# Kernel tuning notes

Measured on AMD Instinct MI355X. Metric: run time of the kernel, lower is better.

Reference implementation:

```python
import jax, jax.numpy as jnp
import numpy as np

B, S, D = 8, 4096, 192
MEM_READ, MEM_WRITE, MEM_READY = 156, 157, 158


def setup_inputs() -> dict:
    key = jax.random.key(0)
    ks = jax.random.split(key, 9)
    inp = {"x": jax.random.normal(ks[0], (B, S, D), dtype=jnp.float32)}
    names = ["Wq_r", "Wk_r", "Wv_r", "Wo_r", "Wq_w", "Wk_w", "Wv_w", "Wo_w"]
    for i, n in enumerate(names):
        inp[n] = jax.random.normal(ks[i + 1], (D, D), dtype=jnp.float32) * 0.02
    return inp


def _attention(x, Wq, Wk, Wv, Wo):
    # single-head, non-causal PureAttention: q/k/v = x @ W.T, softmax(qk^T/sqrt(D)) v, then W_o
    q = jnp.einsum('bsd,ed->bse', x, Wq)
    k = jnp.einsum('bsd,ed->bse', x, Wk)
    v = jnp.einsum('bsd,ed->bse', x, Wv)
    scale = jnp.asarray(1.0 / np.sqrt(D), x.dtype)
    scores = jnp.einsum('bqe,bke->bqk', q, k) * scale  # [B,S,S]
    attn = jax.nn.softmax(scores, axis=-1)
    o = jnp.einsum('bqk,bke->bqe', attn, v)
    return jnp.einsum('bse,oe->bso', o, Wo)


def reference(x, Wq_r, Wk_r, Wv_r, Wo_r, Wq_w, Wk_w, Wv_w, Wo_w):
    read_flag = x[:, 0, MEM_READ]    # [B]
    write_flag = x[:, 0, MEM_WRITE]  # [B]
    read_res = _attention(x, Wq_r, Wk_r, Wv_r, Wo_r)
    write_res = _attention(x, Wq_w, Wk_w, Wv_w, Wo_w)
    rg = read_flag[:, None, None]
    wg = write_flag[:, None, None]
    out = x + rg * (read_res - x) + wg * (write_res - x)
    out = out.at[:, :, MEM_READ].set(0.0)
    out = out.at[:, :, MEM_WRITE].set(0.0)
    ready = (read_flag + write_flag)[:, None]  # broadcast over seq
    out = out.at[:, :, MEM_READY].set(jnp.broadcast_to(ready, out.shape[:2]))
    return out
```

## Files before the change

### kernel.cpp

```cpp
#include <hip/hip_runtime.h>
#include <stdint.h>

#define B_ 8
#define S_ 4096
#define D_ 192
#define M_ (B_*S_)
#define VTILE 13824
#define KTILE 12800
#define NT_ 64

typedef short v8s __attribute__((ext_vector_type(8)));
typedef float v4f __attribute__((ext_vector_type(4)));
typedef unsigned long long ull;

static __device__ __forceinline__ unsigned short f2bf(float f){
  union{float f; unsigned u;} v; v.f=f;
  unsigned u = v.u;
  unsigned r = (u + 0x7fffu + ((u>>16)&1u))>>16;
  return (unsigned short)r;
}
static __device__ __forceinline__ float fexp2(float x){
  return __builtin_amdgcn_exp2f(x);
}

static __device__ __forceinline__ unsigned sw_fp8(float x){
  union{float f; unsigned u;} v; v.f = x;
  unsigned s = (v.u >> 24) & 0x80u;
  float a = fabsf(x);
  if (a < 0.001953125f) return s;
  if (a >= 240.f) return s | 0x7Eu;
  if (a < 0.015625f) {
    int m = (int)(a*512.f + 0.5f); if(m>7) m=7;
    return s | (unsigned)m;
  }
  int e = (int)((v.u >> 23) & 0xff) - 127;
  unsigned mant = (v.u >> 20) & 0x7u;
  unsigned rest = v.u & 0xFFFFFu;
  if (rest > 0x80000u || (rest == 0x80000u && (mant&1u))) mant++;
  unsigned ee = (unsigned)(e + 7);
  if (mant == 8u){ mant = 0u; ee++; }
  return s | (ee<<3) | mant;
}
template<bool HI>
static __device__ __forceinline__ unsigned pk8(float a, float b, unsigned old){
#if __has_builtin(__builtin_amdgcn_cvt_pk_fp8_f32)
  return __builtin_amdgcn_cvt_pk_fp8_f32(a, b, old, HI);
#else
  unsigned p = sw_fp8(a) | (sw_fp8(b)<<8);
  return HI ? ((old & 0x0000FFFFu) | (p<<16)) : ((old & 0xFFFF0000u) | p);
#endif
}

typedef const __attribute__((address_space(1))) unsigned int gu32;
typedef __attribute__((address_space(3))) unsigned int lu32;
#define GLL16(gp, lp) __builtin_amdgcn_global_load_lds((gu32*)(gp), (lu32*)(lp), 16, 0, 0)

__global__ void cvt_w_kernel(const float* w0,const float* w1,const float* w2,const float* w3,
                             const float* w4,const float* w5,const float* w6,const float* w7,
                             unsigned short* dst){
  int w = blockIdx.y;
  const float* src;
  switch(w){
    case 0: src=w0; break; case 1: src=w1; break; case 2: src=w2; break; case 3: src=w3; break;
    case 4: src=w4; break; case 5: src=w5; break; case 6: src=w6; break; default: src=w7; break;
  }
  int i = blockIdx.x*256 + threadIdx.x;
  float v = src[i];
  if(w==0 || w==4 || w==1 || w==5) v *= 0.32267249f;
  dst[(size_t)w*36864 + i] = f2bf(v);
}

__global__ __launch_bounds__(256) void proj_kernel(
    const float* __restrict__ x, const unsigned short* __restrict__ Wb,
    unsigned char* __restrict__ Q8g, unsigned char* __restrict__ K8t,
    unsigned char* __restrict__ V8)
{
  __shared__ __align__(16) unsigned char Vstage8[VTILE];
  const size_t MDB = (size_t)M_*D_;
  int path = blockIdx.y;
  int tid = threadIdx.x;
  int wid = tid>>6, lane = tid&63;
  int lr = lane&15, lg = lane>>4, kb = lg*8;
  int m0 = blockIdx.x*64 + wid*16;
  int row = m0 + lr;

  v8s a[6];
  #pragma unroll
  for(int c=0;c<6;c++){
    const float* xp = &x[(size_t)row*D_ + c*32 + kb];
    float4 f0 = *(const float4*)xp;
    float4 f1 = *(const float4*)(xp+4);
    v8s t;
    t[0]=(short)f2bf(f0.x); t[1]=(short)f2bf(f0.y); t[2]=(short)f2bf(f0.z); t[3]=(short)f2bf(f0.w);
    t[4]=(short)f2bf(f1.x); t[5]=(short)f2bf(f1.y); t[6]=(short)f2bf(f1.z); t[7]=(short)f2bf(f1.w);
    a[c]=t;
  }
  int bidx = m0 / S_;
  int sb   = (blockIdx.x*64) % S_;
  int tile = sb >> 6;
  int sloc = wid*16 + lg*4;

  {
    const unsigned short* W = Wb + (size_t)(path*4 + 0)*36864;
    unsigned char* dst = Q8g + (size_t)path*MDB;
    #pragma unroll
    for(int nt=0; nt<12; nt++){
      v4f acc = {0.f,0.f,0.f,0.f};
      int n = nt*16 + lr;
      #pragma unroll
      for(int c=0;c<6;c++){
        v8s bfr = *(const v8s*)&W[(size_t)n*D_ + c*32 + kb];
        acc = __builtin_amdgcn_mfma_f32_16x16x32_bf16(a[c], bfr, acc, 0,0,0);
      }
      int col = nt*16 + lr;
      int r0 = m0 + lg*4;
      #pragma unroll
      for(int r=0;r<4;r++){
        unsigned p = pk8<false>(acc[r], 0.f, 0u);
        dst[(size_t)(r0+r)*D_ + col] = (unsigned char)(p & 0xFF);
      }
    }
  }
  {
    const unsigned short* W = Wb + (size_t)(path*4 + 1)*36864;
    unsigned char* dstK = K8t + (((size_t)path*B_ + bidx)*NT_ + tile)*KTILE;
    #pragma unroll
    for(int nt=0; nt<12; nt++){
      v4f acc = {0.f,0.f,0.f,0.f};
      int n = nt*16 + lr;
      #pragma unroll
      for(int c=0;c<6;c++){
        v8s bfr = *(const v8s*)&W[(size_t)n*D_ + c*32 + kb];
        acc = __builtin_amdgcn_mfma_f32_16x16x32_bf16(a[c], bfr, acc, 0,0,0);
      }
      int col = nt*16 + lr;
      #pragma unroll
      for(int r=0;r<4;r++){
        unsigned p = pk8<false>(acc[r], 0.f, 0u);
        dstK[(size_t)(sloc+r)*200 + col] = (unsigned char)(p & 0xFF);
      }
    }
  }
  {
    const unsigned short* W = Wb + (size_t)(path*4 + 2)*36864;
    #pragma unroll
    for(int nt=0; nt<12; nt++){
      v4f acc = {0.f,0.f,0.f,0.f};
      int n = nt*16 + lr;
      #pragma unroll
      for(int c=0;c<6;c++){
        v8s bfr = *(const v8s*)&W[(size_t)n*D_ + c*32 + kb];
        acc = __builtin_amdgcn_mfma_f32_16x16x32_bf16(a[c], bfr, acc, 0,0,0);
      }
      int col = nt*16 + lr;
      unsigned pk4 = pk8<false>(acc[0], acc[1], 0u);
      pk4 = pk8<true>(acc[2], acc[3], pk4);
      *(unsigned*)&Vstage8[col*72 + sloc] = pk4;
    }
    __syncthreads();
    unsigned char* dstV = V8 + (((size_t)path*B_ + bidx)*NT_ + tile)*VTILE;
    #pragma unroll
    for(int j=0;j<4;j++){
      int i = tid + j*256;
      if(i<864) *(v8s*)&dstV[i*16] = *(const v8s*)&Vstage8[i*16];
    }
  }
}

__global__ __launch_bounds__(512,4) void attn_kernel(
    const unsigned char* __restrict__ Q8g,
    const unsigned char* __restrict__ K8t,
    const unsigned char* __restrict__ V8,
    unsigned short* __restrict__ Ob)
{
  __shared__ __align__(16) unsigned char KL[2][KTILE];
  __shared__ __align__(16) unsigned char VL8[3][VTILE];

  int flat = blockIdx.x + 32*blockIdx.y + 256*blockIdx.z;
  int w = (flat&7)*64 + (flat>>3);
  int qi = w & 31;
  int b  = (w>>5) & 7;
  int z  = w>>8;

  const size_t MDB = (size_t)M_*D_;
  const unsigned char* Q8 = Q8g + (size_t)z*MDB;
  const unsigned char* Kp = K8t + ((size_t)z*B_ + b)*NT_*KTILE;
  const unsigned char* Vp = V8 + ((size_t)z*B_ + b)*NT_*VTILE;
  unsigned short* O = Ob + (size_t)z*MDB;

  int q0 = qi*128;
  int tid = threadIdx.x, wid=tid>>6, lane=tid&63;
  int lr = lane&15, lg = lane>>4;
  size_t bK = (size_t)b*S_*D_;
  int qrow0 = q0 + wid*16;

  long qf8[6];
  {
    const unsigned char* qp = Q8 + bK + (size_t)(qrow0 + lr)*D_;
    #pragma unroll
    for(int c=0;c<6;c++) qf8[c] = *(const long*)(qp + c*32 + lg*8);
  }
  float lsum = 0.f;
  v4f oacc[12];
  #pragma unroll
  for(int e=0;e<12;e++) oacc[e] = (v4f){0.f,0.f,0.f,0.f};

  bool k2 = tid < 288;
  bool v2 = tid < 352;

  auto stage = [&](int t, int kbuf, int vbuf){
    const unsigned char* kg = Kp + (size_t)t*KTILE;
    const unsigned char* vg = Vp + (size_t)t*VTILE;
    GLL16(kg + tid*16, &KL[kbuf][tid*16]);
    if(k2) GLL16(kg + (512+tid)*16, &KL[kbuf][(512+tid)*16]);
    GLL16(vg + tid*16, &VL8[vbuf][tid*16]);
    if(v2) GLL16(vg + (512+tid)*16, &VL8[vbuf][(512+tid)*16]);
  };
  auto do_qk = [&](int kcur, v4f sacc[4]){
    __builtin_amdgcn_s_setprio(1);
    #pragma unroll
    for(int ct=0; ct<4; ct++){
      v4f s = {0.f,0.f,0.f,0.f};
      const unsigned char* rb = &KL[kcur][(ct*16+lr)*200];
      #pragma unroll
      for(int c=0;c<6;c++){
        long kf8 = *(const long*)(rb + c*32 + lg*8);
        s = __builtin_amdgcn_mfma_f32_16x16x32_fp8_fp8(kf8, qf8[c], s, 0,0,0);
      }
      sacc[ct]=s;
    }
    __builtin_amdgcn_s_setprio(0);
  };
  auto do_softmax = [&](v4f sacc[4], long pa8[2]){
    #pragma unroll
    for(int h=0; h<2; h++){
      v4f s0 = sacc[2*h], s1 = sacc[2*h+1];
      float p00=fexp2(s0[0]), p01=fexp2(s0[1]), p02=fexp2(s0[2]), p03=fexp2(s0[3]);
      float p10=fexp2(s1[0]), p11=fexp2(s1[1]), p12=fexp2(s1[2]), p13=fexp2(s1[3]);
      lsum += ((p00+p01)+(p02+p03)) + ((p10+p11)+(p12+p13));
      unsigned A = pk8<false>(p00,p01,0u); A = pk8<true>(p02,p03,A);
      unsigned Bx= pk8<false>(p10,p11,0u); Bx= pk8<true>(p12,p13,Bx);
      asm("v_permlane32_swap_b32 %0, %1" : "+v"(Bx), "+v"(A));
      asm("v_permlane16_swap_b32 %0, %1" : "+v"(Bx), "+v"(A));
      pa8[h] = (long)(((ull)Bx<<32) | (ull)A);
    }
  };
  auto do_pv = [&](int vcur, long pa8[2]){
    __builtin_amdgcn_s_setprio(1);
    #pragma unroll
    for(int e=0;e<12;e++){
      const unsigned char* vr = &VL8[vcur][(e*16+lr)*72 + lg*8];
      long vb0 = *(const long*)(vr);
      long vb1 = *(const long*)(vr + 32);
      oacc[e] = __builtin_amdgcn_mfma_f32_16x16x32_fp8_fp8(pa8[0], vb0, oacc[e], 0,0,0);
      oacc[e] = __builtin_amdgcn_mfma_f32_16x16x32_fp8_fp8(pa8[1], vb1, oacc[e], 0,0,0);
    }
    __builtin_amdgcn_s_setprio(0);
  };

  stage(0, 0, 0);
  asm volatile("s_waitcnt vmcnt(0)" ::: "memory");
  __syncthreads();

  long pa_prev[2];
  {
    v4f sacc[4];
    do_qk(0, sacc);
    stage(1, 1, 1);
    __builtin_amdgcn_sched_barrier(0);
    do_softmax(sacc, pa_prev);
    asm volatile("s_waitcnt vmcnt(0)" ::: "memory");
    __syncthreads();
  }

  for(int t=1; t<NT_; t++){
    v4f sacc[4];
    do_qk(t&1, sacc);
    if(t<NT_-1) stage(t+1, (t+1)&1, (t+1)%3);
    __builtin_amdgcn_sched_barrier(0);
    do_pv((t-1)%3, pa_prev);
    do_softmax(sacc, pa_prev);
    asm volatile("s_waitcnt vmcnt(0)" ::: "memory");
    __syncthreads();
  }
  do_pv((NT_-1)%3, pa_prev);

  float ps = lsum;
  ps += __shfl_xor(ps, 16);
  ps += __shfl_xor(ps, 32);
  float iv = 1.0f/ps;
  float invr[4];
  #pragma unroll
  for(int r=0;r<4;r++) invr[r] = __shfl(iv, lg*4+r, 16);
  size_t orow0 = ((size_t)b*S_ + qrow0 + lg*4)*D_;
  #pragma unroll
  for(int e=0;e<12;e++){
    #pragma unroll
    for(int r=0;r<4;r++){
      O[orow0 + (size_t)r*D_ + e*16 + lr] = f2bf(oacc[e][r]*invr[r]);
    }
  }
}

__global__ __launch_bounds__(256) void final_kernel(
  const float* __restrict__ x,
  const unsigned short* __restrict__ Or,
  const unsigned short* __restrict__ Ow,
  const unsigned short* __restrict__ WoR,
  const unsigned short* __restrict__ WoW,
  float* __restrict__ out)
{
  int halfn = blockIdx.y;
  int tid=threadIdx.x, wid=tid>>6, lane=tid&63;
  int lr=lane&15, lg=lane>>4, kb=lg*8;
  int m0 = blockIdx.x*64 + wid*16;
  int arow = m0 + lr;
  v8s ar[6], aw[6];
  #pragma unroll
  for(int c=0;c<6;c++){
    ar[c] = *(const v8s*)&Or[(size_t)arow*D_ + c*32 + kb];
    aw[c] = *(const v8s*)&Ow[(size_t)arow*D_ + c*32 + kb];
  }
  int bidx = m0 / S_;
  float rf = x[(size_t)bidx*S_*D_ + 156];
  float wf = x[(size_t)bidx*S_*D_ + 157];
  #pragma unroll
  for(int ntl=0; ntl<6; ntl++){
    int nt = halfn*6 + ntl;
    v4f accR={0.f,0.f,0.f,0.f}, accW={0.f,0.f,0.f,0.f};
    int n = nt*16 + lr;
    #pragma unroll
    for(int c=0;c<6;c++){
      v8s br = *(const v8s*)&WoR[(size_t)n*D_ + c*32 + kb];
      accR = __builtin_amdgcn_mfma_f32_16x16x32_bf16(ar[c], br, accR,0,0,0);
      v8s bw = *(const v8s*)&WoW[(size_t)n*D_ + c*32 + kb];
      accW = __builtin_amdgcn_mfma_f32_16x16x32_bf16(aw[c], bw, accW,0,0,0);
    }
    #pragma unroll
    for(int r=0;r<4;r++){
      int row = m0 + lg*4 + r;
      int col = nt*16 + lr;
      float xv = x[(size_t)row*D_ + col];
      float val = xv + rf*(accR[r]-xv) + wf*(accW[r]-xv);
      if(col==156||col==157) val = 0.f;
      else if(col==158) val = rf+wf;
      out[(size_t)row*D_ + col] = val;
    }
  }
}

extern "C" void kernel_launch(void* const* d_in, const int* in_sizes, int n_in,
                              void* d_out, int out_size, void* d_ws, size_t ws_size,
                              hipStream_t stream) {
  const float* x = (const float*)d_in[0];
  char* wsb = (char*)d_ws;
  const size_t WSZ = 36864;
  const size_t MDB = (size_t)M_*D_;
  const size_t K8SZ = (size_t)2*B_*NT_*KTILE;
  const size_t V8SZ = (size_t)2*B_*NT_*VTILE;
  unsigned short* Wb  = (unsigned short*)wsb;
  unsigned char*  Q8  = (unsigned char*)(wsb + 8*WSZ*2);
  unsigned char*  K8t = Q8 + 2*MDB;
  unsigned char*  V8  = K8t + K8SZ;
  unsigned short* Ob  = (unsigned short*)(V8 + V8SZ);

  cvt_w_kernel<<<dim3(144,8),256,0,stream>>>(
      (const float*)d_in[1],(const float*)d_in[2],(const float*)d_in[3],(const float*)d_in[4],
      (const float*)d_in[5],(const float*)d_in[6],(const float*)d_in[7],(const float*)d_in[8], Wb);

  proj_kernel<<<dim3(512,2),256,0,stream>>>(x, Wb, Q8, K8t, V8);
  attn_kernel<<<dim3(32,8,2),512,0,stream>>>(Q8, K8t, V8, Ob);
  final_kernel<<<dim3(512,2),256,0,stream>>>(x, Ob, Ob + MDB,
                                             Wb+3*WSZ, Wb+7*WSZ, (float*)d_out);
}
```

Baseline: 288.5 us.

## Triple-buffer K/V tiles with two-ahead prefetch and counted vmcnt waits

Adds a third K shared-memory buffer and prefetches tiles two iterations ahead instead of one. Per-wave counted vmcnt waits let only the older tile's loads complete before the barrier, leaving the newest loads in flight. The loop is also restructured to run QK, softmax and PV for the same tile, dropping the software-pipelined PV lag. This removes the full vmcnt(0) drain each iteration, at the cost of more LDS per block (possible occupancy loss) and less overlap between softmax and MFMA work.

```diff
diff --git a/kernel.cpp b/kernel.cpp
--- a/kernel.cpp
+++ b/kernel.cpp
@@ -173,7 +173,7 @@
     const unsigned char* __restrict__ V8,
     unsigned short* __restrict__ Ob)
 {
-  __shared__ __align__(16) unsigned char KL[2][KTILE];
+  __shared__ __align__(16) unsigned char KL[3][KTILE];
   __shared__ __align__(16) unsigned char VL8[3][VTILE];
 
   int flat = blockIdx.x + 32*blockIdx.y + 256*blockIdx.z;
@@ -208,13 +208,19 @@
   bool k2 = tid < 288;
   bool v2 = tid < 352;
 
-  auto stage = [&](int t, int kbuf, int vbuf){
+  auto wait_counted = [&](){
+    if(wid < 5)       asm volatile("s_waitcnt vmcnt(4)" ::: "memory");
+    else if(wid == 5) asm volatile("s_waitcnt vmcnt(3)" ::: "memory");
+    else              asm volatile("s_waitcnt vmcnt(2)" ::: "memory");
+  };
+
+  auto stage = [&](int t, int buf){
     const unsigned char* kg = Kp + (size_t)t*KTILE;
     const unsigned char* vg = Vp + (size_t)t*VTILE;
-    GLL16(kg + tid*16, &KL[kbuf][tid*16]);
-    if(k2) GLL16(kg + (512+tid)*16, &KL[kbuf][(512+tid)*16]);
-    GLL16(vg + tid*16, &VL8[vbuf][tid*16]);
-    if(v2) GLL16(vg + (512+tid)*16, &VL8[vbuf][(512+tid)*16]);
+    GLL16(kg + tid*16, &KL[buf][tid*16]);
+    if(k2) GLL16(kg + (512+tid)*16, &KL[buf][(512+tid)*16]);
+    GLL16(vg + tid*16, &VL8[buf][tid*16]);
+    if(v2) GLL16(vg + (512+tid)*16, &VL8[buf][(512+tid)*16]);
   };
   auto do_qk = [&](int kcur, v4f sacc[4]){
     __builtin_amdgcn_s_setprio(1);
@@ -258,32 +264,24 @@
     __builtin_amdgcn_s_setprio(0);
   };
 
-  stage(0, 0, 0);
+  stage(0, 0);
   asm volatile("s_waitcnt vmcnt(0)" ::: "memory");
   __syncthreads();
-
-  long pa_prev[2];
-  {
+  stage(1, 1);
+
+  for(int t=0; t<NT_; t++){
+    int cur = t % 3;
     v4f sacc[4];
-    do_qk(0, sacc);
-    stage(1, 1, 1);
+    do_qk(cur, sacc);
+    if(t < NT_-2) stage(t+2, (t+2)%3);
     __builtin_amdgcn_sched_barrier(0);
-    do_softmax(sacc, pa_prev);
-    asm volatile("s_waitcnt vmcnt(0)" ::: "memory");
+    long pa8[2];
+    do_softmax(sacc, pa8);
+    do_pv(cur, pa8);
+    if(t < NT_-2) wait_counted();
+    else          asm volatile("s_waitcnt vmcnt(0)" ::: "memory");
     __syncthreads();
   }
-
-  for(int t=1; t<NT_; t++){
-    v4f sacc[4];
-    do_qk(t&1, sacc);
-    if(t<NT_-1) stage(t+1, (t+1)&1, (t+1)%3);
-    __builtin_amdgcn_sched_barrier(0);
-    do_pv((t-1)%3, pa_prev);
-    do_softmax(sacc, pa_prev);
-    asm volatile("s_waitcnt vmcnt(0)" ::: "memory");
-    __syncthreads();
-  }
-  do_pv((NT_-1)%3, pa_prev);
 
   float ps = lsum;
   ps += __shfl_xor(ps, 16);
```

After: 291.2 us. Within noise of the previous version (+0.9%).
